# Performance work log

Measured on AMD Instinct MI355X. Metric: run time of the kernel, lower is better.

## Reference

```python
import jax, jax.numpy as jnp
import numpy as np

DIM = 2048
KV_DIM = 1024
NUM_HEADS = 16
HEAD_DIM = DIM // NUM_HEADS  # 128
EPS = 1e-6
B, LQ, LKV = 2, 4096, 1024


def _rope_cos_sin(L, d, base=10000.0):
    inv_freq = 1.0 / (base ** (np.arange(0, d, 2, dtype=np.float32) / d))  # [d/2]
    freqs = np.arange(L, dtype=np.float32)[:, None] * inv_freq[None, :]   # [L, d/2]
    emb = np.concatenate([freqs, freqs], axis=-1)                          # [L, d]
    return jnp.asarray(np.cos(emb)), jnp.asarray(np.sin(emb))


def setup_inputs() -> dict:
    key = jax.random.key(0)
    ks = jax.random.split(key, 10)
    x = jax.random.normal(ks[0], (B, LQ, DIM), dtype=jnp.float32)
    y = jax.random.normal(ks[1], (B, LKV, KV_DIM), dtype=jnp.float32)
    xc, xs = _rope_cos_sin(LQ, HEAD_DIM)
    yc, ys = _rope_cos_sin(LKV, HEAD_DIM)
    x_cos = jnp.broadcast_to(xc[None], (B, LQ, HEAD_DIM))
    x_sin = jnp.broadcast_to(xs[None], (B, LQ, HEAD_DIM))
    y_cos = jnp.broadcast_to(yc[None], (B, LKV, HEAD_DIM))
    y_sin = jnp.broadcast_to(ys[None], (B, LKV, HEAD_DIM))
    s = 0.02
    Wq = jax.random.normal(ks[2], (DIM, DIM), dtype=jnp.float32) * s
    Wk = jax.random.normal(ks[3], (DIM, KV_DIM), dtype=jnp.float32) * s
    Wv = jax.random.normal(ks[4], (DIM, KV_DIM), dtype=jnp.float32) * s
    Wo = jax.random.normal(ks[5], (DIM, DIM), dtype=jnp.float32) * s
    bq = jnp.zeros((DIM,), jnp.float32)
    bk = jnp.zeros((DIM,), jnp.float32)
    bv = jnp.zeros((DIM,), jnp.float32)
    bo = jnp.zeros((DIM,), jnp.float32)
    rmsq_w = jnp.ones((DIM,), jnp.float32)
    rmsk_w = jnp.ones((DIM,), jnp.float32)
    ln_w = jnp.ones((KV_DIM,), jnp.float32)
    ln_b = jnp.zeros((KV_DIM,), jnp.float32)
    return dict(x=x, y=y, x_cos=x_cos, x_sin=x_sin, y_cos=y_cos, y_sin=y_sin,
                Wq=Wq, bq=bq, Wk=Wk, bk=bk, Wv=Wv, bv=bv, Wo=Wo, bo=bo,
                rmsq_w=rmsq_w, rmsk_w=rmsk_w, ln_w=ln_w, ln_b=ln_b)


def _rms_norm(t, w, eps=EPS):
    return t * jax.lax.rsqrt(jnp.mean(t * t, axis=-1, keepdims=True) + eps) * w


def _layer_norm(t, w, b, eps=EPS):
    mu = jnp.mean(t, axis=-1, keepdims=True)
    var = jnp.mean(jnp.square(t - mu), axis=-1, keepdims=True)
    return (t - mu) * jax.lax.rsqrt(var + eps) * w + b


def _rotate_half(t):
    d2 = t.shape[-1] // 2
    return jnp.concatenate([-t[..., d2:], t[..., :d2]], axis=-1)


def _apply_rope(t, cos, sin):
    # t: [B, L, H, D]; cos/sin: [B, L, D] -> unsqueeze head dim (unsqueeze_dim=2)
    cos = cos[:, :, None, :]
    sin = sin[:, :, None, :]
    return t * cos + _rotate_half(t) * sin


def _block_forward(x, y, x_cos, x_sin, y_cos, y_sin,
                   Wq, bq, Wk, bk, Wv, bv, Wo, bo,
                   rmsq_w, rmsk_w, ln_w, ln_b):
    Bb, Lq, D = x.shape
    Lk = y.shape[1]
    H, Dh = NUM_HEADS, HEAD_DIM
    # y pre-norm (block-level LayerNorm)
    yn = _layer_norm(y, ln_w, ln_b)
    # projections + RMSNorm on q/k
    q = _rms_norm(x @ Wq.T + bq, rmsq_w)   # [B, Lq, D]
    k = _rms_norm(yn @ Wk.T + bk, rmsk_w)  # [B, Lk, D]
    v = yn @ Wv.T + bv                     # [B, Lk, D]
    # split heads and apply RoPE
    q = _apply_rope(q.reshape(Bb, Lq, H, Dh), x_cos, x_sin)
    k = _apply_rope(k.reshape(Bb, Lk, H, Dh), y_cos, y_sin)
    v = v.reshape(Bb, Lk, H, Dh)
    # non-causal cross attention, scale = 1/sqrt(head_dim)
    scale = 1.0 / jnp.sqrt(jnp.asarray(Dh, q.dtype))
    scores = jnp.einsum('blhd,bmhd->bhlm', q, k) * scale
    probs = jax.nn.softmax(scores, axis=-1)
    out = jnp.einsum('bhlm,bmhd->blhd', probs, v).reshape(Bb, Lq, D)
    return out @ Wo.T + bo


def reference(x, y, x_cos, x_sin, y_cos, y_sin,
              Wq, bq, Wk, bk, Wv, bv, Wo, bo,
              rmsq_w, rmsk_w, ln_w, ln_b):
    return _block_forward(x, y, x_cos, x_sin, y_cos, y_sin,
                          Wq, bq, Wk, bk, Wv, bv, Wo, bo,
                          rmsq_w, rmsk_w, ln_w, ln_b)
```

## Files before the change

### kernel.cpp

```cpp
#include <hip/hip_runtime.h>


typedef __attribute__((ext_vector_type(8))) short    short8;
typedef __attribute__((ext_vector_type(8))) unsigned short ushort8;
typedef __attribute__((ext_vector_type(4))) unsigned short ushort4v;
typedef __attribute__((ext_vector_type(4))) float    f32x4;
typedef __attribute__((ext_vector_type(16))) float   f32x16;
typedef __attribute__((ext_vector_type(4))) unsigned int uint4v;

#define DEV __device__ __forceinline__

DEV unsigned short f2bf(float f) {
  unsigned int u = __builtin_bit_cast(unsigned int, f);
  u += 0x7FFFu + ((u >> 16) & 1u);
  return (unsigned short)(u >> 16);
}
DEV float bf2f(unsigned short h) {
  return __builtin_bit_cast(float, ((unsigned int)h) << 16);
}
DEV unsigned int cvtpk_bf16(float lo, float hi) {
  unsigned int r;
  asm("v_cvt_pk_bf16_f32 %0, %1, %2" : "=v"(r) : "v"(lo), "v"(hi));
  return r;
}
DEV short8 mk8(unsigned a, unsigned b, unsigned c, unsigned d) {
  uint4v t; t.x = a; t.y = b; t.z = c; t.w = d;
  return __builtin_bit_cast(short8, t);
}

DEV void gload_lds16(const void* g, void* l) {
  __builtin_amdgcn_global_load_lds(
      (const __attribute__((address_space(1))) void*)g,
      (__attribute__((address_space(3))) void*)l, 16, 0, 0);
}

__global__ __launch_bounds__(256) void cvt_kernel(const float* __restrict__ in,
                                                  unsigned short* __restrict__ out,
                                                  int n4) {
  int idx = blockIdx.x * 256 + threadIdx.x;
  int stride = gridDim.x * 256;
  for (int i = idx; i < n4; i += stride) {
    float4 v = *(const float4*)(in + (size_t)i * 4);
    ushort4v o;
    o.x = f2bf(v.x); o.y = f2bf(v.y); o.z = f2bf(v.z); o.w = f2bf(v.w);
    *(ushort4v*)(out + (size_t)i * 4) = o;
  }
}

__global__ __launch_bounds__(256) void ln_kernel(const float* __restrict__ y,
                                                 const float* __restrict__ w,
                                                 const float* __restrict__ b,
                                                 unsigned short* __restrict__ yn) {
  const int row = blockIdx.x;
  const int t = threadIdx.x;
  const float* yr = y + (size_t)row * 1024;
  float4 v = *(const float4*)(yr + t * 4);
  float s1 = v.x + v.y + v.z + v.w;
  float s2 = v.x * v.x + v.y * v.y + v.z * v.z + v.w * v.w;
#pragma unroll
  for (int m = 1; m < 64; m <<= 1) {
    s1 += __shfl_xor(s1, m);
    s2 += __shfl_xor(s2, m);
  }
  __shared__ float red[8];
  const int wave = t >> 6, lane = t & 63;
  if (lane == 0) { red[wave] = s1; red[4 + wave] = s2; }
  __syncthreads();
  s1 = red[0] + red[1] + red[2] + red[3];
  s2 = red[4] + red[5] + red[6] + red[7];
  const float mu = s1 * (1.0f / 1024.0f);
  const float var = s2 * (1.0f / 1024.0f) - mu * mu;
  const float rs = rsqrtf(var + 1e-6f);
  ushort4v o;
  o.x = f2bf((v.x - mu) * rs * w[t * 4 + 0] + b[t * 4 + 0]);
  o.y = f2bf((v.y - mu) * rs * w[t * 4 + 1] + b[t * 4 + 1]);
  o.z = f2bf((v.z - mu) * rs * w[t * 4 + 2] + b[t * 4 + 2]);
  o.w = f2bf((v.w - mu) * rs * w[t * 4 + 3] + b[t * 4 + 3]);
  *(ushort4v*)(yn + (size_t)row * 1024 + t * 4) = o;
}

__global__ __launch_bounds__(256) void gemm_bt(const unsigned short* __restrict__ A,
                                               const unsigned short* __restrict__ W,
                                               const float* __restrict__ bias0,
                                               const float* __restrict__ bias1,
                                               int nsplit,
                                               unsigned short* __restrict__ Cout,
                                               int M, int N, int K) {
  __shared__ __align__(16) char sA[128 * 128];
  __shared__ __align__(16) char sB[128 * 128];
  const int tid = threadIdx.x;
  const int wave = tid >> 6, lane = tid & 63;
  const int lg = lane >> 4, l15 = lane & 15;
  const int wr = wave >> 1, wc = wave & 1;
  const int m0 = blockIdx.y * 128;
  const int n0 = blockIdx.x * 128;
  const char* Ab = (const char*)A;
  const char* Wb = (const char*)W;
  const size_t ldab = (size_t)K * 2;

  f32x4 acc[4][4] = {};

  for (int kt = 0; kt < K; kt += 64) {
#pragma unroll
    for (int i = 0; i < 4; ++i) {
      const int p = (i * 256 + tid) * 16;
      const int row = p >> 7;
      const int si = (p & 127) ^ ((row & 7) << 4);
      gload_lds16(Ab + (size_t)(m0 + row) * ldab + (size_t)kt * 2 + si, sA + p);
    }
#pragma unroll
    for (int i = 0; i < 4; ++i) {
      const int p = (i * 256 + tid) * 16;
      const int row = p >> 7;
      const int si = (p & 127) ^ ((row & 7) << 4);
      gload_lds16(Wb + (size_t)(n0 + row) * ldab + (size_t)kt * 2 + si, sB + p);
    }
    __syncthreads();
#pragma unroll
    for (int ks = 0; ks < 2; ++ks) {
      const int kb = (ks * 32 + lg * 8) * 2;
      short8 af[4], bw[4];
#pragma unroll
      for (int mf = 0; mf < 4; ++mf) {
        const int row = wr * 64 + mf * 16 + l15;
        af[mf] = *(const short8*)(sA + row * 128 + (kb ^ ((row & 7) << 4)));
      }
#pragma unroll
      for (int nf = 0; nf < 4; ++nf) {
        const int row = wc * 64 + nf * 16 + l15;
        bw[nf] = *(const short8*)(sB + row * 128 + (kb ^ ((row & 7) << 4)));
      }
#pragma unroll
      for (int mf = 0; mf < 4; ++mf)
#pragma unroll
        for (int nf = 0; nf < 4; ++nf)
          acc[mf][nf] = __builtin_amdgcn_mfma_f32_16x16x32_bf16(af[mf], bw[nf],
                                                                acc[mf][nf], 0, 0, 0);
    }
    __syncthreads();
  }

#pragma unroll
  for (int nf = 0; nf < 4; ++nf) {
    const int n = n0 + wc * 64 + nf * 16 + l15;
    const float bv = (n < nsplit) ? bias0[n] : bias1[n - nsplit];
#pragma unroll
    for (int mf = 0; mf < 4; ++mf) {
      const int mB = m0 + wr * 64 + mf * 16 + lg * 4;
#pragma unroll
      for (int r = 0; r < 4; ++r)
        Cout[(size_t)(mB + r) * N + n] = f2bf(acc[mf][nf][r] + bv);
    }
  }
}

template <int EPI>
__global__ __launch_bounds__(512, 2) void gemm256(const unsigned short* __restrict__ A,
                                                  const unsigned short* __restrict__ W,
                                                  const float* __restrict__ bias,
                                                  void* __restrict__ Cout,
                                                  int M, int N, int K) {
  __shared__ __align__(16) char lds[2][4][16384];
  const int tid = threadIdx.x;
  const int wave = tid >> 6, lane = tid & 63;
  const int lg = lane >> 4, l15 = lane & 15;
  const int wm = wave >> 2, wn = wave & 3;

  const int nwg = gridDim.x;
  const int wgid = (blockIdx.x & 7) * (nwg >> 3) + (blockIdx.x >> 3);
  const int nbn = N >> 8;
  const int m0 = (wgid / nbn) * 256;
  const int n0 = (wgid % nbn) * 256;

  const char* Ab = (const char*)A;
  const char* Wb = (const char*)W;
  const size_t ld = (size_t)K * 2;
  const int NT = K >> 6;
  const int NI = NT >> 1;

  const int prow = tid >> 3;
  const int psw  = ((tid * 16) & 127) ^ ((prow & 7) << 4);
  const int pdst = tid * 16;
  const char* pAg = Ab + (size_t)(m0 + prow) * ld + psw;
  const char* pBg = Wb + (size_t)(n0 + prow) * ld + psw;

  f32x4 acc[8][4] = {};
  short8 af[4][2];
  short8 bf[4][2];

#define STG(BUF, HALF, ISB, TAU) do {                                         \
    const char* _g = ((ISB) ? pBg : pAg) + (size_t)(HALF) * 128 * ld +        \
                     (size_t)(TAU) * 128;                                     \
    char* _l = lds[BUF][(ISB) * 2 + (HALF)];                                  \
    gload_lds16(_g, _l + pdst);                                               \
    gload_lds16(_g + 64 * ld, _l + pdst + 8192);                              \
  } while (0)

#define LDA(BUF, H) do {                                                      \
    const char* _b = lds[BUF][wm];                                            \
    _Pragma("unroll") for (int mfl = 0; mfl < 4; ++mfl) {                     \
      const int _r = (H) * 64 + mfl * 16 + l15;                               \
      _Pragma("unroll") for (int ks = 0; ks < 2; ++ks)                        \
        af[mfl][ks] = *(const short8*)(_b + _r * 128 +                        \
                        ((ks * 64 + lg * 16) ^ ((_r & 7) << 4)));             \
    }                                                                         \
  } while (0)

#define LDB(BUF, G) do {                                                      \
    const char* _b = lds[BUF][2 + (wn >> 1)];                                 \
    _Pragma("unroll") for (int nfl = 0; nfl < 2; ++nfl) {                     \
      const int _r = (wn & 1) * 64 + (G) * 32 + nfl * 16 + l15;               \
      _Pragma("unroll") for (int ks = 0; ks < 2; ++ks)                        \
        bf[(G) * 2 + nfl][ks] = *(const short8*)(_b + _r * 128 +              \
                        ((ks * 64 + lg * 16) ^ ((_r & 7) << 4)));             \
    }                                                                         \
  } while (0)

#define MFMA_Q(H, G) do {                                                     \
    __builtin_amdgcn_s_setprio(1);                                            \
    _Pragma("unroll") for (int ks = 0; ks < 2; ++ks)                          \
    _Pragma("unroll") for (int mfl = 0; mfl < 4; ++mfl)                       \
    _Pragma("unroll") for (int nfl = 0; nfl < 2; ++nfl)                       \
      acc[(H) * 4 + mfl][(G) * 2 + nfl] =                                     \
        __builtin_amdgcn_mfma_f32_16x16x32_bf16(af[mfl][ks],                  \
            bf[(G) * 2 + nfl][ks], acc[(H) * 4 + mfl][(G) * 2 + nfl], 0,0,0); \
    __builtin_amdgcn_s_setprio(0);                                            \
  } while (0)

#define BAR() __builtin_amdgcn_s_barrier()
#define LGKM0() do { asm volatile("s_waitcnt lgkmcnt(0)" ::: "memory");       \
    __builtin_amdgcn_sched_barrier(0); } while (0)
#define VM4() asm volatile("s_waitcnt vmcnt(4)" ::: "memory")
#define VM0() asm volatile("s_waitcnt vmcnt(0)" ::: "memory")

  STG(0, 0, 0, 0); STG(0, 1, 0, 0); STG(0, 0, 1, 0); STG(0, 1, 1, 0);
  STG(1, 0, 1, 1); STG(1, 1, 1, 1);
  VM4(); BAR();

  for (int t = 0; t < NI - 1; ++t) {
    const int t2 = 2 * t;
    LDA(0, 0); LDB(0, 0); STG(1, 0, 0, t2 + 1);
    BAR(); LGKM0(); MFMA_Q(0, 0); BAR();
    LDB(0, 1); STG(1, 1, 0, t2 + 1);
    BAR(); LGKM0(); MFMA_Q(0, 1); BAR();
    LDA(0, 1); STG(0, 0, 1, t2 + 2);
    BAR(); LGKM0(); MFMA_Q(1, 1); BAR();
    STG(0, 1, 1, t2 + 2);
    BAR(); MFMA_Q(1, 0); VM4(); BAR();
    LDA(1, 0); LDB(1, 0); STG(0, 0, 0, t2 + 2);
    BAR(); LGKM0(); MFMA_Q(0, 0); BAR();
    LDB(1, 1); STG(0, 1, 0, t2 + 2);
    BAR(); LGKM0(); MFMA_Q(0, 1); BAR();
    LDA(1, 1); STG(1, 0, 1, t2 + 3);
    BAR(); LGKM0(); MFMA_Q(1, 1); BAR();
    STG(1, 1, 1, t2 + 3);
    BAR(); MFMA_Q(1, 0); VM4(); BAR();
  }

  LDA(0, 0); LDB(0, 0); STG(1, 0, 0, NT - 1);
  BAR(); LGKM0(); MFMA_Q(0, 0); BAR();
  LDB(0, 1); STG(1, 1, 0, NT - 1);
  BAR(); LGKM0(); MFMA_Q(0, 1); BAR();
  LDA(0, 1);
  BAR(); LGKM0(); MFMA_Q(1, 1); BAR();
  BAR(); MFMA_Q(1, 0); VM0(); BAR();
  LDA(1, 0); LDB(1, 0); LGKM0(); MFMA_Q(0, 0);
  LDB(1, 1); LGKM0(); MFMA_Q(0, 1);
  LDA(1, 1); LGKM0(); MFMA_Q(1, 1);
  MFMA_Q(1, 0);

#undef STG
#undef LDA
#undef LDB
#undef MFMA_Q
#undef BAR
#undef LGKM0
#undef VM4
#undef VM0

#pragma unroll
  for (int nf = 0; nf < 4; ++nf) {
    const int n = n0 + wn * 64 + nf * 16 + l15;
    const float bv = bias[n];
#pragma unroll
    for (int mf = 0; mf < 8; ++mf) {
      const int mB = m0 + wm * 128 + mf * 16 + lg * 4;
#pragma unroll
      for (int r = 0; r < 4; ++r) {
        const float v = acc[mf][nf][r] + bv;
        if constexpr (EPI == 0)
          ((unsigned short*)Cout)[(size_t)(mB + r) * N + n] = f2bf(v);
        else
          ((float*)Cout)[(size_t)(mB + r) * N + n] = v;
      }
    }
  }
}

__global__ __launch_bounds__(256) void rmsrope_kernel(const unsigned short* __restrict__ in,
                                                      const float* __restrict__ w,
                                                      const float* __restrict__ cs,
                                                      const float* __restrict__ sn,
                                                      unsigned short* __restrict__ out,
                                                      int L, int ldin, float scale) {
  const int row = blockIdx.x;
  const int t = threadIdx.x;
  __shared__ __align__(16) unsigned short srow[2048];
  __shared__ float red[4];
  const unsigned short* ir = in + (size_t)row * ldin;
  ushort8 v = *(const ushort8*)(ir + t * 8);
  float vals[8];
  float ss = 0.f;
#pragma unroll
  for (int j = 0; j < 8; ++j) { vals[j] = bf2f(v[j]); ss += vals[j] * vals[j]; }
  *(ushort8*)(srow + t * 8) = v;
#pragma unroll
  for (int m = 1; m < 64; m <<= 1) ss += __shfl_xor(ss, m);
  const int wave = t >> 6, lane = t & 63;
  if (lane == 0) red[wave] = ss;
  __syncthreads();
  const float tot = red[0] + red[1] + red[2] + red[3];
  const float rms = rsqrtf(tot * (1.0f / 2048.0f) + 1e-6f);

  const int n0 = t * 8;
  const int d0 = n0 & 127;
  const int hh = n0 >> 7;
  const float sign = (d0 < 64) ? -1.0f : 1.0f;
  const float* cb = cs + (size_t)row * 128 + d0;
  const float* sb = sn + (size_t)row * 128 + d0;
  ushort8 po = *(const ushort8*)(srow + (n0 ^ 64));
  ushort8 ou;
#pragma unroll
  for (int j = 0; j < 8; ++j) {
    const float self = vals[j] * rms * w[n0 + j];
    const float part = bf2f(po[j]) * rms * w[(n0 ^ 64) + j];
    ou[j] = f2bf((self * cb[j] + sign * part * sb[j]) * scale);
  }
  const int b = row / L, l = row - (row / L) * L;
  *(ushort8*)(out + (((size_t)(b * 16 + hh)) * L + l) * 128 + d0) = ou;
}

__global__ __launch_bounds__(256) void vtrans_kernel(const unsigned short* __restrict__ vpre,
                                                     unsigned short* __restrict__ vt,
                                                     int ldv) {
  const int bid = blockIdx.x;
  const int kt = bid & 15, bh = bid >> 4;
  const int h = bh & 15, b = bh >> 4;
  __shared__ unsigned short lt[64][130];
  const int t = threadIdx.x;
  const int i0 = t >> 4, c0 = (t & 15) * 8;
  const unsigned short* src = vpre + ((size_t)(b * 1024 + kt * 64)) * ldv + h * 128;
#pragma unroll
  for (int ii = 0; ii < 4; ++ii) {
    const int i = i0 + ii * 16;
    ushort8 v = *(const ushort8*)(src + (size_t)i * ldv + c0);
#pragma unroll
    for (int j = 0; j < 8; ++j) lt[i][c0 + j] = v[j];
  }
  __syncthreads();
  const int d0 = t >> 3, j0 = (t & 7) * 8;
  unsigned short* dst = vt + (size_t)bh * 128 * 1024 + kt * 64;
#pragma unroll
  for (int dd = 0; dd < 4; ++dd) {
    const int d = d0 + dd * 32;
    ushort8 o;
#pragma unroll
    for (int jj = 0; jj < 8; ++jj) o[jj] = lt[j0 + jj][d];
    *(ushort8*)(dst + (size_t)d * 1024 + j0) = o;
  }
}

__global__ __launch_bounds__(512, 2) void attn_kernel(const unsigned short* __restrict__ q,
                                                      const unsigned short* __restrict__ k,
                                                      const unsigned short* __restrict__ vt,
                                                      unsigned short* __restrict__ ao) {
  __shared__ __align__(16) char sK[2][64 * 256];
  __shared__ __align__(16) char sV[2][64 * 256];

  const int bid0 = blockIdx.x;
  const int bid = (bid0 & 7) * 64 + (bid0 >> 3);
  const int qt = bid & 15, bh = bid >> 4;
  const int tid = threadIdx.x;
  const int wave = tid >> 6, lane = tid & 63;
  const int l31 = lane & 31, hi = lane >> 5;
  const bool hib = (hi != 0);

  const unsigned short* qbase = q + (((size_t)bh * 4096) + qt * 256 + wave * 32) * 128;
  const char* kbase = (const char*)(k + (size_t)bh * 1024 * 128);
  const char* vbase = (const char*)(vt + (size_t)bh * 128 * 1024);

  short8 qb[8];
#pragma unroll
  for (int step = 0; step < 8; ++step)
    qb[step] = *(const short8*)(qbase + (size_t)l31 * 128 + step * 16 + hi * 8);

  f32x16 o[4] = {};
  f32x16 ol = {};
  const short8 vones = mk8(0x3F803F80u, 0x3F803F80u, 0x3F803F80u, 0x3F803F80u);

#define STAGE_KV(BUF, KV0) do {                                              \
    _Pragma("unroll")                                                        \
    for (int i = 0; i < 2; ++i) {                                            \
      const int p = (i * 512 + tid) * 16;                                    \
      const int row = p >> 8;                                                \
      const int si = (p & 255) ^ ((row & 15) << 4);                          \
      gload_lds16(kbase + (size_t)((KV0) + row) * 256 + si, sK[BUF] + p);    \
    }                                                                        \
    _Pragma("unroll")                                                        \
    for (int i = 0; i < 2; ++i) {                                            \
      const int p = (i * 512 + tid) * 16;                                    \
      const int row = p >> 8;                                                \
      const int si = (p & 255) ^ ((row & 15) << 4);                          \
      const int d = 2 * row + (si >> 7);                                     \
      gload_lds16(vbase + (size_t)d * 2048 + (KV0) * 2 + (si & 127),         \
                  sV[BUF] + p);                                              \
    }                                                                        \
  } while (0)

#define SOFTMAX_PV(V, SS, F) do {                                            \
    float p_[16];                                                            \
    _Pragma("unroll") for (int r = 0; r < 16; ++r) p_[r] = exp2f((SS)[r]);   \
    const unsigned w0 = cvtpk_bf16(p_[0], p_[1]),  w1 = cvtpk_bf16(p_[2], p_[3]), \
                   w2 = cvtpk_bf16(p_[4], p_[5]),  w3 = cvtpk_bf16(p_[6], p_[7]), \
                   w4 = cvtpk_bf16(p_[8], p_[9]),  w5 = cvtpk_bf16(p_[10], p_[11]),\
                   w6 = cvtpk_bf16(p_[12], p_[13]),w7 = cvtpk_bf16(p_[14], p_[15]);\
    const unsigned x0 = (unsigned)__shfl_xor((int)(hib ? w0 : w2), 32);      \
    const unsigned x1 = (unsigned)__shfl_xor((int)(hib ? w1 : w3), 32);      \
    const unsigned x2 = (unsigned)__shfl_xor((int)(hib ? w4 : w6), 32);      \
    const unsigned x3 = (unsigned)__shfl_xor((int)(hib ? w5 : w7), 32);      \
    const short8 fr0 = mk8(hib ? x0 : w0, hib ? x1 : w1,                     \
                           hib ? w2 : x0, hib ? w3 : x1);                    \
    const short8 fr1 = mk8(hib ? x2 : w4, hib ? x3 : w5,                     \
                           hib ? w6 : x2, hib ? w7 : x3);                    \
    __builtin_amdgcn_s_setprio(1);                                           \
    _Pragma("unroll") for (int kstep = 0; kstep < 2; ++kstep) {              \
      const short8 pa = kstep ? fr1 : fr0;                                   \
      const int colb = (F) * 64 + kstep * 32 + hi * 16;                      \
      _Pragma("unroll") for (int dt = 0; dt < 4; ++dt) {                     \
        const int vrow = dt * 16 + (l31 >> 1);                               \
        const int inner = (l31 & 1) * 128 + colb;                            \
        short8 vf = *(const short8*)((V) + vrow * 256 +                      \
                                     (inner ^ ((vrow & 15) << 4)));          \
        o[dt] = __builtin_amdgcn_mfma_f32_32x32x16_bf16(pa, vf, o[dt], 0,0,0);\
      }                                                                      \
      ol = __builtin_amdgcn_mfma_f32_32x32x16_bf16(pa, vones, ol, 0, 0, 0);  \
    }                                                                        \
    __builtin_amdgcn_s_setprio(0);                                           \
  } while (0)

#define TILE(BUF) do {                                                       \
    const char* const K = sK[BUF];                                           \
    const char* const V = sV[BUF];                                           \
    f32x16 s0 = {}, s1 = {};                                                 \
    const int ksw = (l31 & 15) << 4;                                         \
    __builtin_amdgcn_s_setprio(1);                                           \
    _Pragma("unroll") for (int step = 0; step < 8; ++step) {                 \
      const int cb2 = step * 32 + hi * 16;                                   \
      short8 kf0 = *(const short8*)(K + l31 * 256 + (cb2 ^ ksw));            \
      short8 kf1 = *(const short8*)(K + (32 + l31) * 256 + (cb2 ^ ksw));     \
      s0 = __builtin_amdgcn_mfma_f32_32x32x16_bf16(kf0, qb[step], s0, 0,0,0);\
      s1 = __builtin_amdgcn_mfma_f32_32x32x16_bf16(kf1, qb[step], s1, 0,0,0);\
    }                                                                        \
    __builtin_amdgcn_s_setprio(0);                                           \
    SOFTMAX_PV(V, s0, 0);                                                    \
    SOFTMAX_PV(V, s1, 1);                                                    \
  } while (0)

  STAGE_KV(0, 0);
  __syncthreads();

#pragma unroll 1
  for (int kt2 = 0; kt2 < 8; ++kt2) {
    STAGE_KV(1, (2 * kt2 + 1) * 64);
    TILE(0);
    __syncthreads();
    if (kt2 < 7) STAGE_KV(0, (2 * kt2 + 2) * 64);
    TILE(1);
    __syncthreads();
  }
#undef STAGE_KV
#undef SOFTMAX_PV
#undef TILE

  const int b = bh >> 4, h = bh & 15;
#pragma unroll
  for (int r = 0; r < 16; ++r) {
    const int crow = (r & 3) + 8 * (r >> 2) + 4 * hi;
    const float inv = 1.0f / ol[r];
    const int qg = qt * 256 + wave * 32 + crow;
    const size_t orow = ((size_t)b * 4096 + qg) * 2048 + h * 128;
#pragma unroll
    for (int dt = 0; dt < 4; ++dt)
      ao[orow + dt * 32 + l31] = f2bf(o[dt][r] * inv);
  }
}

extern "C" void kernel_launch(void* const* d_in, const int* in_sizes, int n_in,
                              void* d_out, int out_size, void* d_ws, size_t ws_size,
                              hipStream_t stream) {
  (void)in_sizes; (void)n_in; (void)out_size; (void)ws_size;
  const float* x      = (const float*)d_in[0];
  const float* y      = (const float*)d_in[1];
  const float* x_cos  = (const float*)d_in[2];
  const float* x_sin  = (const float*)d_in[3];
  const float* y_cos  = (const float*)d_in[4];
  const float* y_sin  = (const float*)d_in[5];
  const float* Wq     = (const float*)d_in[6];
  const float* bq     = (const float*)d_in[7];
  const float* Wk     = (const float*)d_in[8];
  const float* bk     = (const float*)d_in[9];
  const float* Wv     = (const float*)d_in[10];
  const float* bv     = (const float*)d_in[11];
  const float* Wo     = (const float*)d_in[12];
  const float* bo     = (const float*)d_in[13];
  const float* rmsq_w = (const float*)d_in[14];
  const float* rmsk_w = (const float*)d_in[15];
  const float* ln_w   = (const float*)d_in[16];
  const float* ln_b   = (const float*)d_in[17];

  char* ws = (char*)d_ws;
  unsigned short* xb    = (unsigned short*)(ws + 0);
  unsigned short* Wqb   = (unsigned short*)(ws + 33554432);
  unsigned short* Wkb   = (unsigned short*)(ws + 41943040);
  unsigned short* Wvb   = (unsigned short*)(ws + 46137344);
  unsigned short* Wob   = (unsigned short*)(ws + 50331648);
  unsigned short* ynb   = (unsigned short*)(ws + 58720256);
  unsigned short* kvpre = (unsigned short*)(ws + 62914560);
  unsigned short* qpre  = (unsigned short*)(ws + 62914560);
  unsigned short* qr    = (unsigned short*)(ws + 96468992);
  unsigned short* kr    = (unsigned short*)(ws + 130023424);
  unsigned short* vt    = (unsigned short*)(ws + 138412032);
  unsigned short* ao    = xb;

  const float qscale = 1.4426950408889634f * 0.08838834764831843f;

  cvt_kernel<<<2048, 256, 0, stream>>>(x, xb, (2 * 4096 * 2048) / 4);
  cvt_kernel<<<512, 256, 0, stream>>>(Wq, Wqb, (2048 * 2048) / 4);
  cvt_kernel<<<512, 256, 0, stream>>>(Wk, Wkb, (2048 * 1024) / 4);
  cvt_kernel<<<512, 256, 0, stream>>>(Wv, Wvb, (2048 * 1024) / 4);
  cvt_kernel<<<512, 256, 0, stream>>>(Wo, Wob, (2048 * 2048) / 4);
  ln_kernel<<<2048, 256, 0, stream>>>(y, ln_w, ln_b, ynb);

  dim3 gKV(32, 16);
  gemm_bt<<<gKV, 256, 0, stream>>>(ynb, Wkb, bk, bv, 2048, kvpre, 2048, 4096, 1024);
  rmsrope_kernel<<<2048, 256, 0, stream>>>(kvpre, rmsk_w, y_cos, y_sin, kr, 1024, 4096, 1.0f);
  vtrans_kernel<<<512, 256, 0, stream>>>(kvpre + 2048, vt, 4096);

  gemm256<0><<<256, 512, 0, stream>>>(xb, Wqb, bq, qpre, 8192, 2048, 2048);
  rmsrope_kernel<<<8192, 256, 0, stream>>>(qpre, rmsq_w, x_cos, x_sin, qr, 4096, 2048, qscale);

  attn_kernel<<<512, 512, 0, stream>>>(qr, kr, vt, ao);

  gemm256<1><<<256, 512, 0, stream>>>(ao, Wob, bo, (float*)d_out, 8192, 2048, 2048);
}
```

Before: 317.3 us.

## Stage 128-row KV tiles per sync in attention and merge weight conversions

The attention kernel now stages two 64-row K/V sub-tiles per buffer, halving the number of barriers and loop iterations over the KV sequence. The four weight fp32-to-bf16 conversion launches are merged into a single kernel. The intent is to cut synchronisation overhead and launch count. The larger LDS footprint (128KB per block) likely reduces resident blocks per CU, which may lower latency hiding.

Result: faster. 306.7 us (-3.4%).

```diff
diff --git a/kernel.cpp b/kernel.cpp
--- a/kernel.cpp
+++ b/kernel.cpp
@@ -44,6 +44,32 @@
     ushort4v o;
     o.x = f2bf(v.x); o.y = f2bf(v.y); o.z = f2bf(v.z); o.w = f2bf(v.w);
     *(ushort4v*)(out + (size_t)i * 4) = o;
+  }
+}
+
+__global__ __launch_bounds__(256) void cvt4_kernel(const float* __restrict__ s0,
+                                                   const float* __restrict__ s1,
+                                                   const float* __restrict__ s2,
+                                                   const float* __restrict__ s3,
+                                                   unsigned short* __restrict__ d0,
+                                                   unsigned short* __restrict__ d1,
+                                                   unsigned short* __restrict__ d2,
+                                                   unsigned short* __restrict__ d3,
+                                                   int n0, int n1, int n2, int n3) {
+  const int total = n0 + n1 + n2 + n3;
+  int idx = blockIdx.x * 256 + threadIdx.x;
+  const int stride = gridDim.x * 256;
+  for (int i = idx; i < total; i += stride) {
+    int j = i;
+    const float* s; unsigned short* d;
+    if (j < n0) { s = s0; d = d0; }
+    else if ((j -= n0) < n1) { s = s1; d = d1; }
+    else if ((j -= n1) < n2) { s = s2; d = d2; }
+    else { j -= n2; s = s3; d = d3; }
+    float4 v = *(const float4*)(s + (size_t)j * 4);
+    ushort4v o;
+    o.x = f2bf(v.x); o.y = f2bf(v.y); o.z = f2bf(v.z); o.w = f2bf(v.w);
+    *(ushort4v*)(d + (size_t)j * 4) = o;
   }
 }
 
@@ -374,8 +400,8 @@
                                                       const unsigned short* __restrict__ k,
                                                       const unsigned short* __restrict__ vt,
                                                       unsigned short* __restrict__ ao) {
-  __shared__ __align__(16) char sK[2][64 * 256];
-  __shared__ __align__(16) char sV[2][64 * 256];
+  __shared__ __align__(16) char sK[2][2][64 * 256];
+  __shared__ __align__(16) char sV[2][2][64 * 256];
 
   const int bid0 = blockIdx.x;
   const int bid = (bid0 & 7) * 64 + (bid0 >> 3);
@@ -400,20 +426,24 @@
 
 #define STAGE_KV(BUF, KV0) do {                                              \
     _Pragma("unroll")                                                        \
-    for (int i = 0; i < 2; ++i) {                                            \
-      const int p = (i * 512 + tid) * 16;                                    \
-      const int row = p >> 8;                                                \
-      const int si = (p & 255) ^ ((row & 15) << 4);                          \
-      gload_lds16(kbase + (size_t)((KV0) + row) * 256 + si, sK[BUF] + p);    \
-    }                                                                        \
-    _Pragma("unroll")                                                        \
-    for (int i = 0; i < 2; ++i) {                                            \
-      const int p = (i * 512 + tid) * 16;                                    \
-      const int row = p >> 8;                                                \
-      const int si = (p & 255) ^ ((row & 15) << 4);                          \
-      const int d = 2 * row + (si >> 7);                                     \
-      gload_lds16(vbase + (size_t)d * 2048 + (KV0) * 2 + (si & 127),         \
-                  sV[BUF] + p);                                              \
+    for (int sub = 0; sub < 2; ++sub) {                                      \
+      _Pragma("unroll")                                                      \
+      for (int i = 0; i < 2; ++i) {                                          \
+        const int p = (i * 512 + tid) * 16;                                  \
+        const int row = p >> 8;                                              \
+        const int si = (p & 255) ^ ((row & 15) << 4);                        \
+        gload_lds16(kbase + (size_t)((KV0) + sub * 64 + row) * 256 + si,     \
+                    sK[BUF][sub] + p);                                       \
+      }                                                                      \
+      _Pragma("unroll")                                                      \
+      for (int i = 0; i < 2; ++i) {                                          \
+        const int p = (i * 512 + tid) * 16;                                  \
+        const int row = p >> 8;                                              \
+        const int si = (p & 255) ^ ((row & 15) << 4);                        \
+        const int d = 2 * row + (si >> 7);                                   \
+        gload_lds16(vbase + (size_t)d * 2048 + ((KV0) + sub * 64) * 2 +      \
+                    (si & 127), sV[BUF][sub] + p);                           \
+      }                                                                      \
     }                                                                        \
   } while (0)
 
@@ -448,16 +478,14 @@
     __builtin_amdgcn_s_setprio(0);                                           \
   } while (0)
 
-#define TILE(BUF) do {                                                       \
-    const char* const K = sK[BUF];                                           \
-    const char* const V = sV[BUF];                                           \
+#define SUBTILE(K, V) do {                                                   \
     f32x16 s0 = {}, s1 = {};                                                 \
     const int ksw = (l31 & 15) << 4;                                         \
     __builtin_amdgcn_s_setprio(1);                                           \
     _Pragma("unroll") for (int step = 0; step < 8; ++step) {                 \
       const int cb2 = step * 32 + hi * 16;                                   \
-      short8 kf0 = *(const short8*)(K + l31 * 256 + (cb2 ^ ksw));            \
-      short8 kf1 = *(const short8*)(K + (32 + l31) * 256 + (cb2 ^ ksw));     \
+      short8 kf0 = *(const short8*)((K) + l31 * 256 + (cb2 ^ ksw));          \
+      short8 kf1 = *(const short8*)((K) + (32 + l31) * 256 + (cb2 ^ ksw));   \
       s0 = __builtin_amdgcn_mfma_f32_32x32x16_bf16(kf0, qb[step], s0, 0,0,0);\
       s1 = __builtin_amdgcn_mfma_f32_32x32x16_bf16(kf1, qb[step], s1, 0,0,0);\
     }                                                                        \
@@ -466,20 +494,26 @@
     SOFTMAX_PV(V, s1, 1);                                                    \
   } while (0)
 
+#define TILE(BUF) do {                                                       \
+    SUBTILE(sK[BUF][0], sV[BUF][0]);                                         \
+    SUBTILE(sK[BUF][1], sV[BUF][1]);                                         \
+  } while (0)
+
   STAGE_KV(0, 0);
   __syncthreads();
 
 #pragma unroll 1
-  for (int kt2 = 0; kt2 < 8; ++kt2) {
-    STAGE_KV(1, (2 * kt2 + 1) * 64);
+  for (int kt2 = 0; kt2 < 4; ++kt2) {
+    STAGE_KV(1, (2 * kt2 + 1) * 128);
     TILE(0);
     __syncthreads();
-    if (kt2 < 7) STAGE_KV(0, (2 * kt2 + 2) * 64);
+    if (kt2 < 3) STAGE_KV(0, (2 * kt2 + 2) * 128);
     TILE(1);
     __syncthreads();
   }
 #undef STAGE_KV
 #undef SOFTMAX_PV
+#undef SUBTILE
 #undef TILE
 
   const int b = bh >> 4, h = bh & 15;
@@ -535,10 +569,9 @@
   const float qscale = 1.4426950408889634f * 0.08838834764831843f;
 
   cvt_kernel<<<2048, 256, 0, stream>>>(x, xb, (2 * 4096 * 2048) / 4);
-  cvt_kernel<<<512, 256, 0, stream>>>(Wq, Wqb, (2048 * 2048) / 4);
-  cvt_kernel<<<512, 256, 0, stream>>>(Wk, Wkb, (2048 * 1024) / 4);
-  cvt_kernel<<<512, 256, 0, stream>>>(Wv, Wvb, (2048 * 1024) / 4);
-  cvt_kernel<<<512, 256, 0, stream>>>(Wo, Wob, (2048 * 2048) / 4);
+  cvt4_kernel<<<2048, 256, 0, stream>>>(Wq, Wk, Wv, Wo, Wqb, Wkb, Wvb, Wob,
+                                        (2048 * 2048) / 4, (2048 * 1024) / 4,
+                                        (2048 * 1024) / 4, (2048 * 2048) / 4);
   ln_kernel<<<2048, 256, 0, stream>>>(y, ln_w, ln_b, ynb);
 
   dim3 gKV(32, 16);
```

## Double attention Q rows per wave, compute row sums in VALU, fuse weight conversions

Applied to the files above, without the earlier changes.

Each attention wave now handles two 32-row Q groups (512 Q rows per block, 256 blocks). Every K and V fragment read from LDS is shared by two MFMAs, which halves LDS traffic per FLOP. The extra ones-vector MFMA for the softmax denominator is replaced by scalar sums of the exponentials plus a cross-lane shuffle. The four weight-conversion launches are merged into one kernel. In exchange, register pressure roughly doubles for Q fragments and accumulators, which may cause spills under the 512x2 launch bounds, and the grid of 256 blocks may underfill the GPU's CUs.

Measured after the change: 404.0 us. 27.3% more time.

```diff
diff --git a/kernel.cpp b/kernel.cpp
--- a/kernel.cpp
+++ b/kernel.cpp
@@ -44,6 +44,32 @@
     ushort4v o;
     o.x = f2bf(v.x); o.y = f2bf(v.y); o.z = f2bf(v.z); o.w = f2bf(v.w);
     *(ushort4v*)(out + (size_t)i * 4) = o;
+  }
+}
+
+__global__ __launch_bounds__(256) void cvt4_kernel(const float* __restrict__ s0,
+                                                   const float* __restrict__ s1,
+                                                   const float* __restrict__ s2,
+                                                   const float* __restrict__ s3,
+                                                   unsigned short* __restrict__ d0,
+                                                   unsigned short* __restrict__ d1,
+                                                   unsigned short* __restrict__ d2,
+                                                   unsigned short* __restrict__ d3,
+                                                   int n0, int n1, int n2, int n3) {
+  const int total = n0 + n1 + n2 + n3;
+  int idx = blockIdx.x * 256 + threadIdx.x;
+  const int stride = gridDim.x * 256;
+  for (int i = idx; i < total; i += stride) {
+    int j = i;
+    const float* s; unsigned short* d;
+    if (j < n0) { s = s0; d = d0; }
+    else if ((j -= n0) < n1) { s = s1; d = d1; }
+    else if ((j -= n1) < n2) { s = s2; d = d2; }
+    else { j -= n2; s = s3; d = d3; }
+    float4 v = *(const float4*)(s + (size_t)j * 4);
+    ushort4v o;
+    o.x = f2bf(v.x); o.y = f2bf(v.y); o.z = f2bf(v.z); o.w = f2bf(v.w);
+    *(ushort4v*)(d + (size_t)j * 4) = o;
   }
 }
 
@@ -378,25 +404,27 @@
   __shared__ __align__(16) char sV[2][64 * 256];
 
   const int bid0 = blockIdx.x;
-  const int bid = (bid0 & 7) * 64 + (bid0 >> 3);
-  const int qt = bid & 15, bh = bid >> 4;
+  const int bid = (bid0 & 7) * 32 + (bid0 >> 3);
+  const int qt = bid & 7, bh = bid >> 3;
   const int tid = threadIdx.x;
   const int wave = tid >> 6, lane = tid & 63;
   const int l31 = lane & 31, hi = lane >> 5;
   const bool hib = (hi != 0);
 
-  const unsigned short* qbase = q + (((size_t)bh * 4096) + qt * 256 + wave * 32) * 128;
+  const unsigned short* qbase = q + (((size_t)bh * 4096) + qt * 512 + wave * 64) * 128;
   const char* kbase = (const char*)(k + (size_t)bh * 1024 * 128);
   const char* vbase = (const char*)(vt + (size_t)bh * 128 * 1024);
 
-  short8 qb[8];
-#pragma unroll
-  for (int step = 0; step < 8; ++step)
-    qb[step] = *(const short8*)(qbase + (size_t)l31 * 128 + step * 16 + hi * 8);
-
-  f32x16 o[4] = {};
-  f32x16 ol = {};
-  const short8 vones = mk8(0x3F803F80u, 0x3F803F80u, 0x3F803F80u, 0x3F803F80u);
+  short8 qb[2][8];
+#pragma unroll
+  for (int g = 0; g < 2; ++g)
+#pragma unroll
+    for (int step = 0; step < 8; ++step)
+      qb[g][step] = *(const short8*)(qbase + (size_t)(g * 32 + l31) * 128 + step * 16 + hi * 8);
+
+  f32x16 o[2][4] = {};
+  float lsum[2] = {0.f, 0.f};
+  short8 frA[2], frB[2];
 
 #define STAGE_KV(BUF, KV0) do {                                              \
     _Pragma("unroll")                                                        \
@@ -417,9 +445,11 @@
     }                                                                        \
   } while (0)
 
-#define SOFTMAX_PV(V, SS, F) do {                                            \
+#define SM(SS, G) do {                                                       \
     float p_[16];                                                            \
     _Pragma("unroll") for (int r = 0; r < 16; ++r) p_[r] = exp2f((SS)[r]);   \
+    lsum[G] += (((p_[0]+p_[1])+(p_[2]+p_[3])) + ((p_[4]+p_[5])+(p_[6]+p_[7])))\
+             + (((p_[8]+p_[9])+(p_[10]+p_[11])) + ((p_[12]+p_[13])+(p_[14]+p_[15])));\
     const unsigned w0 = cvtpk_bf16(p_[0], p_[1]),  w1 = cvtpk_bf16(p_[2], p_[3]), \
                    w2 = cvtpk_bf16(p_[4], p_[5]),  w3 = cvtpk_bf16(p_[6], p_[7]), \
                    w4 = cvtpk_bf16(p_[8], p_[9]),  w5 = cvtpk_bf16(p_[10], p_[11]),\
@@ -428,42 +458,39 @@
     const unsigned x1 = (unsigned)__shfl_xor((int)(hib ? w1 : w3), 32);      \
     const unsigned x2 = (unsigned)__shfl_xor((int)(hib ? w4 : w6), 32);      \
     const unsigned x3 = (unsigned)__shfl_xor((int)(hib ? w5 : w7), 32);      \
-    const short8 fr0 = mk8(hib ? x0 : w0, hib ? x1 : w1,                     \
-                           hib ? w2 : x0, hib ? w3 : x1);                    \
-    const short8 fr1 = mk8(hib ? x2 : w4, hib ? x3 : w5,                     \
-                           hib ? w6 : x2, hib ? w7 : x3);                    \
-    __builtin_amdgcn_s_setprio(1);                                           \
+    frA[G] = mk8(hib ? x0 : w0, hib ? x1 : w1, hib ? w2 : x0, hib ? w3 : x1);\
+    frB[G] = mk8(hib ? x2 : w4, hib ? x3 : w5, hib ? w6 : x2, hib ? w7 : x3);\
+  } while (0)
+
+#define HALF(K, V, H) do {                                                   \
+    f32x16 s0 = {}, s1 = {};                                                 \
+    const int ksw = (l31 & 15) << 4;                                         \
+    _Pragma("unroll") for (int step = 0; step < 8; ++step) {                 \
+      const int cb2 = step * 32 + hi * 16;                                   \
+      short8 kf = *(const short8*)((K) + ((H) * 32 + l31) * 256 + (cb2 ^ ksw));\
+      s0 = __builtin_amdgcn_mfma_f32_32x32x16_bf16(kf, qb[0][step], s0, 0,0,0);\
+      s1 = __builtin_amdgcn_mfma_f32_32x32x16_bf16(kf, qb[1][step], s1, 0,0,0);\
+    }                                                                        \
+    SM(s0, 0);                                                               \
+    SM(s1, 1);                                                               \
     _Pragma("unroll") for (int kstep = 0; kstep < 2; ++kstep) {              \
-      const short8 pa = kstep ? fr1 : fr0;                                   \
-      const int colb = (F) * 64 + kstep * 32 + hi * 16;                      \
+      const int colb = (H) * 64 + kstep * 32 + hi * 16;                      \
       _Pragma("unroll") for (int dt = 0; dt < 4; ++dt) {                     \
         const int vrow = dt * 16 + (l31 >> 1);                               \
         const int inner = (l31 & 1) * 128 + colb;                            \
         short8 vf = *(const short8*)((V) + vrow * 256 +                      \
                                      (inner ^ ((vrow & 15) << 4)));          \
-        o[dt] = __builtin_amdgcn_mfma_f32_32x32x16_bf16(pa, vf, o[dt], 0,0,0);\
+        o[0][dt] = __builtin_amdgcn_mfma_f32_32x32x16_bf16(                  \
+            kstep ? frB[0] : frA[0], vf, o[0][dt], 0, 0, 0);                 \
+        o[1][dt] = __builtin_amdgcn_mfma_f32_32x32x16_bf16(                  \
+            kstep ? frB[1] : frA[1], vf, o[1][dt], 0, 0, 0);                 \
       }                                                                      \
-      ol = __builtin_amdgcn_mfma_f32_32x32x16_bf16(pa, vones, ol, 0, 0, 0);  \
     }                                                                        \
-    __builtin_amdgcn_s_setprio(0);                                           \
   } while (0)
 
 #define TILE(BUF) do {                                                       \
-    const char* const K = sK[BUF];                                           \
-    const char* const V = sV[BUF];                                           \
-    f32x16 s0 = {}, s1 = {};                                                 \
-    const int ksw = (l31 & 15) << 4;                                         \
-    __builtin_amdgcn_s_setprio(1);                                           \
-    _Pragma("unroll") for (int step = 0; step < 8; ++step) {                 \
-      const int cb2 = step * 32 + hi * 16;                                   \
-      short8 kf0 = *(const short8*)(K + l31 * 256 + (cb2 ^ ksw));            \
-      short8 kf1 = *(const short8*)(K + (32 + l31) * 256 + (cb2 ^ ksw));     \
-      s0 = __builtin_amdgcn_mfma_f32_32x32x16_bf16(kf0, qb[step], s0, 0,0,0);\
-      s1 = __builtin_amdgcn_mfma_f32_32x32x16_bf16(kf1, qb[step], s1, 0,0,0);\
-    }                                                                        \
-    __builtin_amdgcn_s_setprio(0);                                           \
-    SOFTMAX_PV(V, s0, 0);                                                    \
-    SOFTMAX_PV(V, s1, 1);                                                    \
+    HALF(sK[BUF], sV[BUF], 0);                                               \
+    HALF(sK[BUF], sV[BUF], 1);                                               \
   } while (0)
 
   STAGE_KV(0, 0);
@@ -479,19 +506,29 @@
     __syncthreads();
   }
 #undef STAGE_KV
-#undef SOFTMAX_PV
+#undef SM
+#undef HALF
 #undef TILE
 
+  float linv[2];
+#pragma unroll
+  for (int g = 0; g < 2; ++g) {
+    float t = lsum[g] + __shfl_xor(lsum[g], 32);
+    linv[g] = 1.0f / t;
+  }
   const int b = bh >> 4, h = bh & 15;
 #pragma unroll
-  for (int r = 0; r < 16; ++r) {
-    const int crow = (r & 3) + 8 * (r >> 2) + 4 * hi;
-    const float inv = 1.0f / ol[r];
-    const int qg = qt * 256 + wave * 32 + crow;
-    const size_t orow = ((size_t)b * 4096 + qg) * 2048 + h * 128;
-#pragma unroll
-    for (int dt = 0; dt < 4; ++dt)
-      ao[orow + dt * 32 + l31] = f2bf(o[dt][r] * inv);
+  for (int g = 0; g < 2; ++g) {
+#pragma unroll
+    for (int r = 0; r < 16; ++r) {
+      const int crow = (r & 3) + 8 * (r >> 2) + 4 * hi;
+      const float inv = __shfl(linv[g], crow);
+      const int qg = qt * 512 + wave * 64 + g * 32 + crow;
+      const size_t orow = ((size_t)b * 4096 + qg) * 2048 + h * 128;
+#pragma unroll
+      for (int dt = 0; dt < 4; ++dt)
+        ao[orow + dt * 32 + l31] = f2bf(o[g][dt][r] * inv);
+    }
   }
 }
 
@@ -535,10 +572,9 @@
   const float qscale = 1.4426950408889634f * 0.08838834764831843f;
 
   cvt_kernel<<<2048, 256, 0, stream>>>(x, xb, (2 * 4096 * 2048) / 4);
-  cvt_kernel<<<512, 256, 0, stream>>>(Wq, Wqb, (2048 * 2048) / 4);
-  cvt_kernel<<<512, 256, 0, stream>>>(Wk, Wkb, (2048 * 1024) / 4);
-  cvt_kernel<<<512, 256, 0, stream>>>(Wv, Wvb, (2048 * 1024) / 4);
-  cvt_kernel<<<512, 256, 0, stream>>>(Wo, Wob, (2048 * 2048) / 4);
+  cvt4_kernel<<<2048, 256, 0, stream>>>(Wq, Wk, Wv, Wo, Wqb, Wkb, Wvb, Wob,
+                                        (2048 * 2048) / 4, (2048 * 1024) / 4,
+                                        (2048 * 1024) / 4, (2048 * 2048) / 4);
   ln_kernel<<<2048, 256, 0, stream>>>(y, ln_w, ln_b, ynb);
 
   dim3 gKV(32, 16);
@@ -549,7 +585,7 @@
   gemm256<0><<<256, 512, 0, stream>>>(xb, Wqb, bq, qpre, 8192, 2048, 2048);
   rmsrope_kernel<<<8192, 256, 0, stream>>>(qpre, rmsq_w, x_cos, x_sin, qr, 4096, 2048, qscale);
 
-  attn_kernel<<<512, 512, 0, stream>>>(qr, kr, vt, ao);
+  attn_kernel<<<256, 512, 0, stream>>>(qr, kr, vt, ao);
 
   gemm256<1><<<256, 512, 0, stream>>>(ao, Wob, bo, (float*)d_out, 8192, 2048, 2048);
 }
```
